# Performance work log

Measured on AMD Instinct MI355X. Metric: run time of the kernel, lower is better.

## Reference

```python
import jax, jax.numpy as jnp
import numpy as np

N = 50000   # num nodes
E = 800000  # num edges (avg degree 16)
D = 128     # in = hidden = out channels


def setup_inputs() -> dict:
    key = jax.random.key(0)
    k0, k1, k2, k3, k4, k5 = jax.random.split(key, 6)
    x = jax.random.normal(k0, (N, D), dtype=jnp.float32)
    edge_index = jax.random.randint(k1, (2, E), 0, N, dtype=jnp.int32)
    scale = 1.0 / np.sqrt(D)
    W1 = jax.random.normal(k2, (D, D), dtype=jnp.float32) * scale
    b1 = jax.random.normal(k3, (D,), dtype=jnp.float32) * 0.01
    W2 = jax.random.normal(k4, (D, D), dtype=jnp.float32) * scale
    b2 = jax.random.normal(k5, (D,), dtype=jnp.float32) * 0.01
    return {"x": x, "edge_index": edge_index, "W1": W1, "b1": b1, "W2": W2, "b2": b2}


def reference(x, edge_index, W1, b1, W2, b2):
    n = x.shape[0]
    src, dst = edge_index[0], edge_index[1]
    # GCN adds self-loops before normalization
    loops = jnp.arange(n, dtype=src.dtype)
    s = jnp.concatenate([src, loops])
    d = jnp.concatenate([dst, loops])
    # symmetric normalization: deg^{-1/2}[s] * deg^{-1/2}[d]
    deg = jax.ops.segment_sum(jnp.ones_like(d, dtype=x.dtype), d, num_segments=n)
    dinv = jnp.where(deg > 0, jax.lax.rsqrt(deg), 0.0)
    ew = dinv[s] * dinv[d]  # [E+N]

    def gcn_conv(h, W, b):
        h = h @ W                                   # [N, D] dense transform first
        msg = ew[:, None] * h[s]                     # gather over edges [E+N, D]
        agg = jax.ops.segment_sum(msg, d, num_segments=n)  # scatter-add [N, D]
        return agg + b

    # layer 1: conv -> Identity BN -> ELU (dropout=0.0 -> no-op)
    h = jax.nn.elu(gcn_conv(x, W1, b1))
    # layer 2 (last): conv -> Identity BN -> ELU
    out = jax.nn.elu(gcn_conv(h, W2, b2))
    return out
```

## Files before the change

kernel.cpp:

```cpp
#include <hip/hip_runtime.h>
#include <math.h>

#define D 128
#define BCAP 8192
#define SLICE 64
#define PB 256

typedef __attribute__((ext_vector_type(8))) short bf16x8;
typedef __attribute__((ext_vector_type(4))) float f32x4;


__device__ inline float2 bf2f2(unsigned int u) {
    union { unsigned int i; float f; } a, b;
    a.i = u << 16;
    b.i = u & 0xffff0000u;
    return make_float2(a.f, b.f);
}

__device__ inline unsigned short f2bf(float f) {
    union { float f; unsigned int i; } u;
    u.f = f;
    unsigned int r = u.i + 0x7fffu + ((u.i >> 16) & 1u);
    return (unsigned short)(r >> 16);
}


__device__ __forceinline__ void gemm_core(unsigned short (*Ws)[136], int gbid,
                                          const void* __restrict__ Ain, int a_fp32,
                                          unsigned int* __restrict__ Cb, int N) {
    const int tid = threadIdx.x;
    const int wid = tid >> 6;
    const int lane = tid & 63;
    const int quad = lane >> 4;
    const int ln = lane & 15;
    const int m = gbid * 64 + wid * 16 + ln;
    const bool valid = (m < N);

    f32x4 acc[8];
#pragma unroll
    for (int c = 0; c < 8; ++c) acc[c] = (f32x4){0.f, 0.f, 0.f, 0.f};

    __syncthreads();

#pragma unroll
    for (int ks = 0; ks < 4; ++ks) {
        const int k0 = ks * 32;
        bf16x8 af;
        if (a_fp32) {
            const float* A = (const float*)Ain;
            float4 lo = make_float4(0.f, 0.f, 0.f, 0.f), hi = lo;
            if (valid) {
                lo = *(const float4*)&A[(size_t)m * 128 + k0 + quad * 8];
                hi = *(const float4*)&A[(size_t)m * 128 + k0 + quad * 8 + 4];
            }
            af[0] = (short)f2bf(lo.x); af[1] = (short)f2bf(lo.y);
            af[2] = (short)f2bf(lo.z); af[3] = (short)f2bf(lo.w);
            af[4] = (short)f2bf(hi.x); af[5] = (short)f2bf(hi.y);
            af[6] = (short)f2bf(hi.z); af[7] = (short)f2bf(hi.w);
        } else {
            const uint4* A4 = (const uint4*)Ain;
            uint4 v = valid ? A4[(size_t)m * 16 + ks * 4 + quad]
                            : make_uint4(0u, 0u, 0u, 0u);
            union { uint4 u; bf16x8 h; } cv;
            cv.u = v;
            af = cv.h;
        }
#pragma unroll
        for (int c = 0; c < 8; ++c) {
            bf16x8 bf = *(const bf16x8*)&Ws[c * 16 + ln][k0 + quad * 8];
            acc[c] = __builtin_amdgcn_mfma_f32_16x16x32_bf16(af, bf, acc[c], 0, 0, 0);
        }
    }

    const int rowbase = gbid * 64 + wid * 16 + quad * 4;
#pragma unroll
    for (int c = 0; c < 8; ++c) {
#pragma unroll
        for (int r = 0; r < 4; ++r) {
            float v = acc[c][r];
            float vn = __shfl_xor(v, 1);
            int grow = rowbase + r;
            if (!(ln & 1) && grow < N) {
                unsigned int u = (unsigned int)f2bf(v) | ((unsigned int)f2bf(vn) << 16);
                Cb[(size_t)grow * 64 + c * 8 + (ln >> 1)] = u;
            }
        }
    }
}


__global__ __launch_bounds__(256) void k1_all(
        const int* __restrict__ src, const int* __restrict__ dst,
        const float* __restrict__ x, const float* __restrict__ W1,
        const float* __restrict__ W2, unsigned short* __restrict__ Wt2,
        unsigned int* __restrict__ pairs, unsigned char* __restrict__ cellCnt,
        unsigned int* __restrict__ hb1, int e, int chunk, int N, int gemmBlocks) {
    __shared__ __align__(16) unsigned char smem[128 * 136 * 2];
    const int tid = threadIdx.x;
    const int bid = blockIdx.x;

    if (bid < PB) {
        int* cur = (int*)smem;
        cur[tid] = 0;
        __syncthreads();
        const int e0 = bid * chunk;
        const int e1 = min(e0 + chunk, e);
        for (int i = e0 + tid; i < e1; i += 256) {
            int d = dst[i], s = src[i];
            int b = d >> 8;
            int off = atomicAdd(&cur[b], 1);
            if (off < SLICE)
                pairs[((size_t)(bid * 256 + b)) * SLICE + off] =
                    (unsigned int)s | ((unsigned int)(d & 255) << 16);
        }
        __syncthreads();
        cellCnt[bid * 256 + tid] = (unsigned char)min(cur[tid], SLICE);
    } else if (bid < PB + gemmBlocks) {
        unsigned short (*Ws)[136] = (unsigned short(*)[136])smem;
        for (int j = 0; j < 64; ++j) {
            int idx = tid + j * 256;
            Ws[idx & 127][idx >> 7] = f2bf(W1[idx]);
        }
        gemm_core(Ws, bid - PB, x, 1, hb1, N);
    } else {
        int i = (bid - PB - gemmBlocks) * 256 + tid;
        int k = i >> 7, n = i & 127;
        Wt2[n * 128 + k] = f2bf(W2[i]);
    }
}


__global__ __launch_bounds__(256) void partB(const unsigned int* __restrict__ pairs,
                                             const unsigned char* __restrict__ cellCnt,
                                             unsigned short* __restrict__ col,
                                             unsigned int* __restrict__ meta,
                                             float* __restrict__ dinv, int n) {
    __shared__ int deg[256];
    __shared__ int sc[256];
    __shared__ int cur[256];
    const int b = blockIdx.x;
    const int tid = threadIdx.x;

    deg[tid] = 0;
    __syncthreads();

    const int c = cellCnt[tid * 256 + b];
    const unsigned int* cell = pairs + ((size_t)(tid * 256 + b)) * SLICE;
    for (int q = 0; q < c; ++q) atomicAdd(&deg[cell[q] >> 16], 1);
    __syncthreads();

    int v = deg[tid];
    sc[tid] = v;
    __syncthreads();
    for (int o = 1; o < 256; o <<= 1) {
        int t = (tid >= o) ? sc[tid - o] : 0;
        __syncthreads();
        sc[tid] += t;
        __syncthreads();
    }
    int startw = sc[tid] - v;
    cur[tid] = startw;

    int node = b * 256 + tid;
    if (node < n) {
        meta[node] = ((unsigned int)(b * BCAP + startw) << 10) | (unsigned int)v;
        dinv[node] = rsqrtf((float)(v + 1));
    }
    __syncthreads();

    for (int q = 0; q < c; ++q) {
        unsigned int p = cell[q];
        int dl = p >> 16;
        int off = atomicAdd(&cur[dl], 1);
        col[(size_t)b * BCAP + off] = (unsigned short)(p & 0xffffu);
    }
}


__device__ __forceinline__ float2 agg_node(const unsigned int* __restrict__ hb,
                                           const unsigned int* __restrict__ meta,
                                           const unsigned short* __restrict__ col,
                                           const float* __restrict__ dinv,
                                           int node, int lane, float2 bv) {
    const float di = dinv[node];
    float2 self = bf2f2(hb[(size_t)node * 64 + lane]);
    float2 a0 = make_float2(di * self.x, di * self.y);
    float2 a1 = make_float2(0.f, 0.f), a2 = make_float2(0.f, 0.f),
           a3 = make_float2(0.f, 0.f), a4 = make_float2(0.f, 0.f),
           a5 = make_float2(0.f, 0.f), a6 = make_float2(0.f, 0.f),
           a7 = make_float2(0.f, 0.f);

    const unsigned int m = meta[node];
    const int s0 = (int)(m >> 10);
    const int s1 = s0 + (int)(m & 1023u);
    int i = s0;
    for (; i + 8 <= s1; i += 8) {
        int c0 = col[i + 0], c1 = col[i + 1], c2 = col[i + 2], c3 = col[i + 3];
        int c4 = col[i + 4], c5 = col[i + 5], c6 = col[i + 6], c7 = col[i + 7];
        float w0 = dinv[c0], w1 = dinv[c1], w2 = dinv[c2], w3 = dinv[c3];
        float w4 = dinv[c4], w5 = dinv[c5], w6 = dinv[c6], w7 = dinv[c7];
        unsigned int u0 = hb[(size_t)c0 * 64 + lane];
        unsigned int u1 = hb[(size_t)c1 * 64 + lane];
        unsigned int u2 = hb[(size_t)c2 * 64 + lane];
        unsigned int u3 = hb[(size_t)c3 * 64 + lane];
        unsigned int u4 = hb[(size_t)c4 * 64 + lane];
        unsigned int u5 = hb[(size_t)c5 * 64 + lane];
        unsigned int u6 = hb[(size_t)c6 * 64 + lane];
        unsigned int u7 = hb[(size_t)c7 * 64 + lane];
        float2 v0 = bf2f2(u0), v1 = bf2f2(u1), v2 = bf2f2(u2), v3 = bf2f2(u3);
        float2 v4 = bf2f2(u4), v5 = bf2f2(u5), v6 = bf2f2(u6), v7 = bf2f2(u7);
        a0.x = fmaf(w0, v0.x, a0.x); a0.y = fmaf(w0, v0.y, a0.y);
        a1.x = fmaf(w1, v1.x, a1.x); a1.y = fmaf(w1, v1.y, a1.y);
        a2.x = fmaf(w2, v2.x, a2.x); a2.y = fmaf(w2, v2.y, a2.y);
        a3.x = fmaf(w3, v3.x, a3.x); a3.y = fmaf(w3, v3.y, a3.y);
        a4.x = fmaf(w4, v4.x, a4.x); a4.y = fmaf(w4, v4.y, a4.y);
        a5.x = fmaf(w5, v5.x, a5.x); a5.y = fmaf(w5, v5.y, a5.y);
        a6.x = fmaf(w6, v6.x, a6.x); a6.y = fmaf(w6, v6.y, a6.y);
        a7.x = fmaf(w7, v7.x, a7.x); a7.y = fmaf(w7, v7.y, a7.y);
    }
    for (; i < s1; ++i) {
        int c = col[i];
        float ww = dinv[c];
        float2 v = bf2f2(hb[(size_t)c * 64 + lane]);
        a0.x = fmaf(ww, v.x, a0.x); a0.y = fmaf(ww, v.y, a0.y);
    }

    float sx = (a0.x + a1.x) + (a2.x + a3.x) + (a4.x + a5.x) + (a6.x + a7.x);
    float sy = (a0.y + a1.y) + (a2.y + a3.y) + (a4.y + a5.y) + (a6.y + a7.y);
    float rx = fmaf(di, sx, bv.x);
    float ry = fmaf(di, sy, bv.y);
    rx = rx > 0.0f ? rx : expm1f(rx);
    ry = ry > 0.0f ? ry : expm1f(ry);
    return make_float2(rx, ry);
}


__global__ __launch_bounds__(256) void k3_agg_gemm(
        const unsigned int* __restrict__ hb1, const unsigned int* __restrict__ meta,
        const unsigned short* __restrict__ col, const float* __restrict__ dinv,
        const float* __restrict__ b1, const unsigned short* __restrict__ Wt2,
        unsigned int* __restrict__ hb2, int n) {
    __shared__ unsigned int g1s[16 * 68];
    __shared__ __align__(16) unsigned short Ws[64][136];

    const int tid = threadIdx.x;
    const int wid = tid >> 6;
    const int lane = tid & 63;
    const int nodeBase = blockIdx.x * 16;
    const float2 bv = ((const float2*)b1)[lane];

    for (int t = 0; t < 4; ++t) {
        const int node = nodeBase + wid * 4 + t;
        unsigned int packed = 0;
        if (node < n) {
            float2 r = agg_node(hb1, meta, col, dinv, node, lane, bv);
            packed = (unsigned int)f2bf(r.x) | ((unsigned int)f2bf(r.y) << 16);
        }
        g1s[(wid * 4 + t) * 68 + lane] = packed;
    }
    __syncthreads();

    const int quad = lane >> 4;
    const int ln = lane & 15;

#pragma unroll
    for (int pass = 0; pass < 2; ++pass) {
        {
            int nloc = tid >> 2;
            int kb = (tid & 3) * 32;
            const uint4* g = (const uint4*)(Wt2 + (size_t)(pass * 64 + nloc) * 128 + kb);
            uint4* s = (uint4*)&Ws[nloc][kb];
            s[0] = g[0]; s[1] = g[1]; s[2] = g[2]; s[3] = g[3];
        }
        __syncthreads();

        f32x4 acc = (f32x4){0.f, 0.f, 0.f, 0.f};
#pragma unroll
        for (int ks = 0; ks < 4; ++ks) {
            bf16x8 af = *(const bf16x8*)&g1s[ln * 68 + ks * 16 + quad * 4];
            bf16x8 bf = *(const bf16x8*)&Ws[wid * 16 + ln][ks * 32 + quad * 8];
            acc = __builtin_amdgcn_mfma_f32_16x16x32_bf16(af, bf, acc, 0, 0, 0);
        }
        const int c = pass * 4 + wid;
#pragma unroll
        for (int r = 0; r < 4; ++r) {
            float v = acc[r];
            float vn = __shfl_xor(v, 1);
            int grow = nodeBase + quad * 4 + r;
            if (!(ln & 1) && grow < n) {
                hb2[(size_t)grow * 64 + c * 8 + (ln >> 1)] =
                    (unsigned int)f2bf(v) | ((unsigned int)f2bf(vn) << 16);
            }
        }
        __syncthreads();
    }
}


__global__ __launch_bounds__(256) void agg_elu(const unsigned int* __restrict__ hb,
                                               const unsigned int* __restrict__ meta,
                                               const unsigned short* __restrict__ col,
                                               const float* __restrict__ dinv,
                                               const float* __restrict__ bias,
                                               float* __restrict__ outf, int n) {
    const int wid = threadIdx.x >> 6;
    const int lane = threadIdx.x & 63;
    const int node = blockIdx.x * 4 + wid;
    if (node >= n) return;
    const float2 bv = ((const float2*)bias)[lane];
    float2 r = agg_node(hb, meta, col, dinv, node, lane, bv);
    ((float2*)outf)[(size_t)node * 64 + lane] = r;
}


extern "C" void kernel_launch(void* const* d_in, const int* in_sizes, int n_in,
                              void* d_out, int out_size, void* d_ws, size_t ws_size,
                              hipStream_t stream) {
    const float* x  = (const float*)d_in[0];
    const int*   ei = (const int*)d_in[1];
    const float* W1 = (const float*)d_in[2];
    const float* b1 = (const float*)d_in[3];
    const float* W2 = (const float*)d_in[4];
    const float* b2 = (const float*)d_in[5];
    float* out = (float*)d_out;

    const int N = in_sizes[0] / D;
    const int E = in_sizes[1] / 2;
    const int* src = ei;
    const int* dst = ei + E;
    const int NB = (N + 255) / 256;

    char* ws = (char*)d_ws;
    size_t off = 0;
    auto alloc = [&](size_t bytes) -> void* {
        void* p = ws + off;
        off = (off + bytes + 255) & ~(size_t)255;
        return p;
    };
    unsigned int*   pairs   = (unsigned int*)alloc((size_t)PB * 256 * SLICE * 4);
    unsigned char*  cellCnt = (unsigned char*)alloc((size_t)PB * 256);
    unsigned short* col     = (unsigned short*)alloc((size_t)NB * BCAP * 2);
    unsigned int*   meta    = (unsigned int*)alloc((size_t)N * 4);
    float*          dinv    = (float*)alloc((size_t)N * 4);
    unsigned short* Wt2     = (unsigned short*)alloc(128 * 128 * 2);
    unsigned int*   hb1     = (unsigned int*)alloc((size_t)N * 64 * 4);
    unsigned int*   hb2     = (unsigned int*)alloc((size_t)N * 64 * 4);
    (void)ws_size; (void)n_in; (void)out_size;

    const int chunk = (E + PB - 1) / PB;
    const int gemmBlocks = (N + 63) / 64;

    k1_all<<<PB + gemmBlocks + 64, 256, 0, stream>>>(src, dst, x, W1, W2, Wt2,
                                                     pairs, cellCnt, hb1, E, chunk,
                                                     N, gemmBlocks);
    partB<<<NB, 256, 0, stream>>>(pairs, cellCnt, col, meta, dinv, N);
    k3_agg_gemm<<<(N + 15) / 16, 256, 0, stream>>>(hb1, meta, col, dinv, b1, Wt2, hb2, N);
    agg_elu<<<(N + 3) / 4, 256, 0, stream>>>(hb2, meta, col, dinv, b2, out, N);
}
```

Measured before the change: 199.3 us.

## Split each wavefront into two half-waves gathering alternate neighbors with 8-byte loads

The neighbor aggregation now has each half-wavefront (32 lanes) handle alternate edges. Each lane loads 8 bytes (4 bf16 features) per neighbor row, and the two halves are combined with a cross-half shuffle at the end. This doubles the number of independent neighbor rows in flight per wave and widens each load, aiming to cut latency-bound gather time. The fused kernel also vector-loads meta and dinv for its four nodes up front, and both kernels get an occupancy hint of 6 blocks. The risks are extra shuffle and lane-permutation work and a more complex remainder loop.

Result: slower. 214.5 us (+7.6%).

```diff
diff --git a/kernel.cpp b/kernel.cpp
--- a/kernel.cpp
+++ b/kernel.cpp
@@ -177,56 +177,82 @@
 }
 
 
+__device__ __forceinline__ f32x4 fma4(float w, uint2 u, f32x4 a) {
+    float2 f0 = bf2f2(u.x), f1 = bf2f2(u.y);
+    a[0] = fmaf(w, f0.x, a[0]);
+    a[1] = fmaf(w, f0.y, a[1]);
+    a[2] = fmaf(w, f1.x, a[2]);
+    a[3] = fmaf(w, f1.y, a[3]);
+    return a;
+}
+
 __device__ __forceinline__ float2 agg_node(const unsigned int* __restrict__ hb,
-                                           const unsigned int* __restrict__ meta,
                                            const unsigned short* __restrict__ col,
                                            const float* __restrict__ dinv,
-                                           int node, int lane, float2 bv) {
-    const float di = dinv[node];
-    float2 self = bf2f2(hb[(size_t)node * 64 + lane]);
-    float2 a0 = make_float2(di * self.x, di * self.y);
-    float2 a1 = make_float2(0.f, 0.f), a2 = make_float2(0.f, 0.f),
-           a3 = make_float2(0.f, 0.f), a4 = make_float2(0.f, 0.f),
-           a5 = make_float2(0.f, 0.f), a6 = make_float2(0.f, 0.f),
-           a7 = make_float2(0.f, 0.f);
-
-    const unsigned int m = meta[node];
+                                           int node, int lane, float2 bv,
+                                           unsigned int m, float di) {
+    const int ph = lane >> 5;
+    const int l5 = lane & 31;
     const int s0 = (int)(m >> 10);
     const int s1 = s0 + (int)(m & 1023u);
+
+    f32x4 a0, a1, a2, a3;
+    {
+        uint2 su = *(const uint2*)&hb[(size_t)node * 64 + (l5 << 1)];
+        float2 f0 = bf2f2(su.x), f1 = bf2f2(su.y);
+        float ws = ph ? 0.f : di;
+        a0 = (f32x4){ws * f0.x, ws * f0.y, ws * f1.x, ws * f1.y};
+    }
+    a1 = (f32x4){0.f, 0.f, 0.f, 0.f};
+    a2 = a1;
+    a3 = a1;
+
     int i = s0;
-    for (; i + 8 <= s1; i += 8) {
-        int c0 = col[i + 0], c1 = col[i + 1], c2 = col[i + 2], c3 = col[i + 3];
-        int c4 = col[i + 4], c5 = col[i + 5], c6 = col[i + 6], c7 = col[i + 7];
+    for (; i + 16 <= s1; i += 16) {
+        int c0 = col[i + 0 + ph], c1 = col[i + 2 + ph];
+        int c2 = col[i + 4 + ph], c3 = col[i + 6 + ph];
+        int c4 = col[i + 8 + ph], c5 = col[i + 10 + ph];
+        int c6 = col[i + 12 + ph], c7 = col[i + 14 + ph];
         float w0 = dinv[c0], w1 = dinv[c1], w2 = dinv[c2], w3 = dinv[c3];
         float w4 = dinv[c4], w5 = dinv[c5], w6 = dinv[c6], w7 = dinv[c7];
-        unsigned int u0 = hb[(size_t)c0 * 64 + lane];
-        unsigned int u1 = hb[(size_t)c1 * 64 + lane];
-        unsigned int u2 = hb[(size_t)c2 * 64 + lane];
-        unsigned int u3 = hb[(size_t)c3 * 64 + lane];
-        unsigned int u4 = hb[(size_t)c4 * 64 + lane];
-        unsigned int u5 = hb[(size_t)c5 * 64 + lane];
-        unsigned int u6 = hb[(size_t)c6 * 64 + lane];
-        unsigned int u7 = hb[(size_t)c7 * 64 + lane];
-        float2 v0 = bf2f2(u0), v1 = bf2f2(u1), v2 = bf2f2(u2), v3 = bf2f2(u3);
-        float2 v4 = bf2f2(u4), v5 = bf2f2(u5), v6 = bf2f2(u6), v7 = bf2f2(u7);
-        a0.x = fmaf(w0, v0.x, a0.x); a0.y = fmaf(w0, v0.y, a0.y);
-        a1.x = fmaf(w1, v1.x, a1.x); a1.y = fmaf(w1, v1.y, a1.y);
-        a2.x = fmaf(w2, v2.x, a2.x); a2.y = fmaf(w2, v2.y, a2.y);
-        a3.x = fmaf(w3, v3.x, a3.x); a3.y = fmaf(w3, v3.y, a3.y);
-        a4.x = fmaf(w4, v4.x, a4.x); a4.y = fmaf(w4, v4.y, a4.y);
-        a5.x = fmaf(w5, v5.x, a5.x); a5.y = fmaf(w5, v5.y, a5.y);
-        a6.x = fmaf(w6, v6.x, a6.x); a6.y = fmaf(w6, v6.y, a6.y);
-        a7.x = fmaf(w7, v7.x, a7.x); a7.y = fmaf(w7, v7.y, a7.y);
-    }
-    for (; i < s1; ++i) {
-        int c = col[i];
-        float ww = dinv[c];
-        float2 v = bf2f2(hb[(size_t)c * 64 + lane]);
-        a0.x = fmaf(ww, v.x, a0.x); a0.y = fmaf(ww, v.y, a0.y);
-    }
-
-    float sx = (a0.x + a1.x) + (a2.x + a3.x) + (a4.x + a5.x) + (a6.x + a7.x);
-    float sy = (a0.y + a1.y) + (a2.y + a3.y) + (a4.y + a5.y) + (a6.y + a7.y);
+        uint2 u0 = *(const uint2*)&hb[(size_t)c0 * 64 + (l5 << 1)];
+        uint2 u1 = *(const uint2*)&hb[(size_t)c1 * 64 + (l5 << 1)];
+        uint2 u2 = *(const uint2*)&hb[(size_t)c2 * 64 + (l5 << 1)];
+        uint2 u3 = *(const uint2*)&hb[(size_t)c3 * 64 + (l5 << 1)];
+        uint2 u4 = *(const uint2*)&hb[(size_t)c4 * 64 + (l5 << 1)];
+        uint2 u5 = *(const uint2*)&hb[(size_t)c5 * 64 + (l5 << 1)];
+        uint2 u6 = *(const uint2*)&hb[(size_t)c6 * 64 + (l5 << 1)];
+        uint2 u7 = *(const uint2*)&hb[(size_t)c7 * 64 + (l5 << 1)];
+        a0 = fma4(w0, u0, a0); a1 = fma4(w1, u1, a1);
+        a2 = fma4(w2, u2, a2); a3 = fma4(w3, u3, a3);
+        a0 = fma4(w4, u4, a0); a1 = fma4(w5, u5, a1);
+        a2 = fma4(w6, u6, a2); a3 = fma4(w7, u7, a3);
+    }
+    int rem = s1 - i;
+    if (rem > 0) {
+#pragma unroll
+        for (int j = 0; j < 8; ++j) {
+            int tt = 2 * j + ph;
+            if (tt < rem) {
+                int cc = col[i + tt];
+                float ww = dinv[cc];
+                uint2 uu = *(const uint2*)&hb[(size_t)cc * 64 + (l5 << 1)];
+                if ((j & 3) == 0)      a0 = fma4(ww, uu, a0);
+                else if ((j & 3) == 1) a1 = fma4(ww, uu, a1);
+                else if ((j & 3) == 2) a2 = fma4(ww, uu, a2);
+                else                   a3 = fma4(ww, uu, a3);
+            }
+        }
+    }
+
+    f32x4 s = (a0 + a1) + (a2 + a3);
+    s[0] += __shfl_xor(s[0], 32);
+    s[1] += __shfl_xor(s[1], 32);
+    s[2] += __shfl_xor(s[2], 32);
+    s[3] += __shfl_xor(s[3], 32);
+
+    float sx = ph ? s[2] : s[0];
+    float sy = ph ? s[3] : s[1];
     float rx = fmaf(di, sx, bv.x);
     float ry = fmaf(di, sy, bv.y);
     rx = rx > 0.0f ? rx : expm1f(rx);
@@ -235,7 +261,7 @@
 }
 
 
-__global__ __launch_bounds__(256) void k3_agg_gemm(
+__global__ __launch_bounds__(256, 6) void k3_agg_gemm(
         const unsigned int* __restrict__ hb1, const unsigned int* __restrict__ meta,
         const unsigned short* __restrict__ col, const float* __restrict__ dinv,
         const float* __restrict__ b1, const unsigned short* __restrict__ Wt2,
@@ -246,17 +272,37 @@
     const int tid = threadIdx.x;
     const int wid = tid >> 6;
     const int lane = tid & 63;
+    const int ph = lane >> 5;
+    const int l5 = lane & 31;
     const int nodeBase = blockIdx.x * 16;
-    const float2 bv = ((const float2*)b1)[lane];
-
+    const float2 bv = ((const float2*)b1)[(l5 << 1) + ph];
+
+    const int nb = nodeBase + wid * 4;
+    unsigned int m4[4];
+    float d4[4];
+    if (nb + 3 < n) {
+        const uint4 mv = *(const uint4*)&meta[nb];
+        const float4 dv = *(const float4*)&dinv[nb];
+        m4[0] = mv.x; m4[1] = mv.y; m4[2] = mv.z; m4[3] = mv.w;
+        d4[0] = dv.x; d4[1] = dv.y; d4[2] = dv.z; d4[3] = dv.w;
+    } else {
+#pragma unroll
+        for (int t = 0; t < 4; ++t) {
+            const int nd = nb + t;
+            m4[t] = (nd < n) ? meta[nd] : 0u;
+            d4[t] = (nd < n) ? dinv[nd] : 0.f;
+        }
+    }
+
+#pragma unroll
     for (int t = 0; t < 4; ++t) {
-        const int node = nodeBase + wid * 4 + t;
+        const int node = nb + t;
         unsigned int packed = 0;
         if (node < n) {
-            float2 r = agg_node(hb1, meta, col, dinv, node, lane, bv);
+            float2 r = agg_node(hb1, col, dinv, node, lane, bv, m4[t], d4[t]);
             packed = (unsigned int)f2bf(r.x) | ((unsigned int)f2bf(r.y) << 16);
         }
-        g1s[(wid * 4 + t) * 68 + lane] = packed;
+        g1s[(wid * 4 + t) * 68 + (l5 << 1) + ph] = packed;
     }
     __syncthreads();
 
@@ -297,19 +343,23 @@
 }
 
 
-__global__ __launch_bounds__(256) void agg_elu(const unsigned int* __restrict__ hb,
-                                               const unsigned int* __restrict__ meta,
-                                               const unsigned short* __restrict__ col,
-                                               const float* __restrict__ dinv,
-                                               const float* __restrict__ bias,
-                                               float* __restrict__ outf, int n) {
+__global__ __launch_bounds__(256, 6) void agg_elu(const unsigned int* __restrict__ hb,
+                                                  const unsigned int* __restrict__ meta,
+                                                  const unsigned short* __restrict__ col,
+                                                  const float* __restrict__ dinv,
+                                                  const float* __restrict__ bias,
+                                                  float* __restrict__ outf, int n) {
     const int wid = threadIdx.x >> 6;
     const int lane = threadIdx.x & 63;
+    const int ph = lane >> 5;
+    const int l5 = lane & 31;
     const int node = blockIdx.x * 4 + wid;
     if (node >= n) return;
-    const float2 bv = ((const float2*)bias)[lane];
-    float2 r = agg_node(hb, meta, col, dinv, node, lane, bv);
-    ((float2*)outf)[(size_t)node * 64 + lane] = r;
+    const float2 bv = ((const float2*)bias)[(l5 << 1) + ph];
+    const unsigned int m = meta[node];
+    const float di = dinv[node];
+    float2 r = agg_node(hb, col, dinv, node, lane, bv, m, di);
+    ((float2*)outf)[(size_t)node * 64 + (l5 << 1) + ph] = r;
 }
 
 
```

## Use 1024-thread blocks in agg-gemm kernel with one node per wave

Applied to the files above, without the earlier changes.

Restructures the fused aggregation+GEMM kernel to launch 16 waves per block, one per node, instead of 4 waves each aggregating 4 nodes serially. The full 128x128 W2 tile is loaded into shared memory once, and 8 waves run the MFMA for all output columns in a single pass, removing the two-pass loop and its extra barriers. The intent is more memory-level parallelism in the latency-bound gather. The cost is larger LDS per block, half the waves idle during the GEMM, and possible register pressure under the launch_bounds(1024, 8) hint.

Result: no change. 201.5 us (+1.1%).

```diff
diff --git a/kernel.cpp b/kernel.cpp
--- a/kernel.cpp
+++ b/kernel.cpp
@@ -178,11 +178,10 @@
 
 
 __device__ __forceinline__ float2 agg_node(const unsigned int* __restrict__ hb,
-                                           const unsigned int* __restrict__ meta,
                                            const unsigned short* __restrict__ col,
                                            const float* __restrict__ dinv,
-                                           int node, int lane, float2 bv) {
-    const float di = dinv[node];
+                                           int node, int lane, float2 bv,
+                                           unsigned int m, float di) {
     float2 self = bf2f2(hb[(size_t)node * 64 + lane]);
     float2 a0 = make_float2(di * self.x, di * self.y);
     float2 a1 = make_float2(0.f, 0.f), a2 = make_float2(0.f, 0.f),
@@ -190,7 +189,6 @@
            a5 = make_float2(0.f, 0.f), a6 = make_float2(0.f, 0.f),
            a7 = make_float2(0.f, 0.f);
 
-    const unsigned int m = meta[node];
     const int s0 = (int)(m >> 10);
     const int s1 = s0 + (int)(m & 1023u);
     int i = s0;
@@ -235,45 +233,43 @@
 }
 
 
-__global__ __launch_bounds__(256) void k3_agg_gemm(
+__global__ __launch_bounds__(1024, 8) void k3_agg_gemm(
         const unsigned int* __restrict__ hb1, const unsigned int* __restrict__ meta,
         const unsigned short* __restrict__ col, const float* __restrict__ dinv,
         const float* __restrict__ b1, const unsigned short* __restrict__ Wt2,
         unsigned int* __restrict__ hb2, int n) {
     __shared__ unsigned int g1s[16 * 68];
-    __shared__ __align__(16) unsigned short Ws[64][136];
+    __shared__ __align__(16) unsigned short Ws[128][136];
 
     const int tid = threadIdx.x;
     const int wid = tid >> 6;
     const int lane = tid & 63;
     const int nodeBase = blockIdx.x * 16;
+    const int node = nodeBase + wid;
+
+    {
+        const int nloc = tid >> 3;
+        const int kb = (tid & 7) * 16;
+        const uint4* g = (const uint4*)(Wt2 + (size_t)nloc * 128 + kb);
+        uint4* s = (uint4*)&Ws[nloc][kb];
+        s[0] = g[0];
+        s[1] = g[1];
+    }
+
     const float2 bv = ((const float2*)b1)[lane];
-
-    for (int t = 0; t < 4; ++t) {
-        const int node = nodeBase + wid * 4 + t;
-        unsigned int packed = 0;
-        if (node < n) {
-            float2 r = agg_node(hb1, meta, col, dinv, node, lane, bv);
-            packed = (unsigned int)f2bf(r.x) | ((unsigned int)f2bf(r.y) << 16);
-        }
-        g1s[(wid * 4 + t) * 68 + lane] = packed;
-    }
-    __syncthreads();
-
-    const int quad = lane >> 4;
-    const int ln = lane & 15;
-
-#pragma unroll
-    for (int pass = 0; pass < 2; ++pass) {
-        {
-            int nloc = tid >> 2;
-            int kb = (tid & 3) * 32;
-            const uint4* g = (const uint4*)(Wt2 + (size_t)(pass * 64 + nloc) * 128 + kb);
-            uint4* s = (uint4*)&Ws[nloc][kb];
-            s[0] = g[0]; s[1] = g[1]; s[2] = g[2]; s[3] = g[3];
-        }
-        __syncthreads();
-
+    unsigned int packed = 0;
+    if (node < n) {
+        const unsigned int m = meta[node];
+        const float di = dinv[node];
+        float2 r = agg_node(hb1, col, dinv, node, lane, bv, m, di);
+        packed = (unsigned int)f2bf(r.x) | ((unsigned int)f2bf(r.y) << 16);
+    }
+    g1s[wid * 68 + lane] = packed;
+    __syncthreads();
+
+    if (wid < 8) {
+        const int quad = lane >> 4;
+        const int ln = lane & 15;
         f32x4 acc = (f32x4){0.f, 0.f, 0.f, 0.f};
 #pragma unroll
         for (int ks = 0; ks < 4; ++ks) {
@@ -281,18 +277,16 @@
             bf16x8 bf = *(const bf16x8*)&Ws[wid * 16 + ln][ks * 32 + quad * 8];
             acc = __builtin_amdgcn_mfma_f32_16x16x32_bf16(af, bf, acc, 0, 0, 0);
         }
-        const int c = pass * 4 + wid;
 #pragma unroll
         for (int r = 0; r < 4; ++r) {
             float v = acc[r];
             float vn = __shfl_xor(v, 1);
             int grow = nodeBase + quad * 4 + r;
             if (!(ln & 1) && grow < n) {
-                hb2[(size_t)grow * 64 + c * 8 + (ln >> 1)] =
+                hb2[(size_t)grow * 64 + wid * 8 + (ln >> 1)] =
                     (unsigned int)f2bf(v) | ((unsigned int)f2bf(vn) << 16);
             }
         }
-        __syncthreads();
     }
 }
 
@@ -308,7 +302,9 @@
     const int node = blockIdx.x * 4 + wid;
     if (node >= n) return;
     const float2 bv = ((const float2*)bias)[lane];
-    float2 r = agg_node(hb, meta, col, dinv, node, lane, bv);
+    const unsigned int m = meta[node];
+    const float di = dinv[node];
+    float2 r = agg_node(hb, col, dinv, node, lane, bv, m, di);
     ((float2*)outf)[(size_t)node * 64 + lane] = r;
 }
 
@@ -354,6 +350,6 @@
                                                      pairs, cellCnt, hb1, E, chunk,
                                                      N, gemmBlocks);
     partB<<<NB, 256, 0, stream>>>(pairs, cellCnt, col, meta, dinv, N);
-    k3_agg_gemm<<<(N + 15) / 16, 256, 0, stream>>>(hb1, meta, col, dinv, b1, Wt2, hb2, N);
+    k3_agg_gemm<<<(N + 15) / 16, 1024, 0, stream>>>(hb1, meta, col, dinv, b1, Wt2, hb2, N);
     agg_elu<<<(N + 3) / 4, 256, 0, stream>>>(hb2, meta, col, dinv, b2, out, N);
 }
```
